# Kernel optimization log

Measured on AMD Instinct MI355X. Metric: run time of the kernel, lower is better.

The kernel has to match this reference:

```python
import jax, jax.numpy as jnp
import numpy as np
import math

M = 0.4      # angular margin
S = 64.0     # scale
K = 0.7      # virtual-prototype damping
START_VP_EPOCH = 4


def _l2norm(v, eps):
    # F.normalize: v / max(||v||_2, eps), row-wise
    n = jnp.sqrt(jnp.sum(v * v, axis=-1, keepdims=True))
    return v / jnp.maximum(n, eps)


def setup_inputs() -> dict:
    key = jax.random.key(0)
    k1, k2, k3, k4 = jax.random.split(key, 4)
    B, D, C = 256, 512, 100000
    return {
        "x": jax.random.normal(k1, (B, D), dtype=jnp.float32),
        "labels": jax.random.randint(k2, (B,), 0, C),
        "weight": jax.random.normal(k3, (C, D), dtype=jnp.float32) * 0.05,
        "queue": jax.random.normal(k4, (C, D), dtype=jnp.float32),
        "epoch": 5,
    }


def reference(x, labels, weight, queue, epoch):
    labels = labels.astype(jnp.int32)
    C = weight.shape[0]

    emb = _l2norm(x, 1e-5)                                   # [B, D]
    cosine = emb @ _l2norm(weight, 1e-5).T                   # [B, C]
    cosine = jnp.clip(cosine, -1.0 + 1e-7, 1.0 - 1e-7)

    # --- update_virtual_prototype (fully detached in the original) ---
    emb_d = jax.lax.stop_gradient(emb)
    q_rows = queue[labels]                                   # [B, D] gather
    # diag(queue[labels] @ emb.T) == rowwise dot (avoid O(B^2) matmul)
    drift = jnp.sum(q_rows * emb_d, axis=1)                  # [B]
    factor = (drift / (1.0 + jnp.abs(drift)))[:, None]       # softsign
    new_rows = _l2norm(factor * q_rows + (1.0 - factor) * emb_d, 1e-12)
    queue = queue.at[labels].set(new_rows)

    if epoch + 1 >= START_VP_EPOCH:
        qn = jax.lax.stop_gradient(_l2norm(queue, 1e-12))    # [C, D]
        vp_sim = emb @ qn.T                                  # [B, C]
        B = vp_sim.shape[0]
        rows = jnp.arange(B)
        diag = vp_sim[rows, labels]
        # v - k * v.detach()  ->  value (1-k)*v, grad passes as identity
        vp_sim = vp_sim.at[rows, labels].set(diag - K * jax.lax.stop_gradient(diag))
        cosine = jnp.concatenate([cosine, vp_sim], axis=0)   # [2B, C]
        labels = jnp.concatenate([labels, labels], axis=0)

    one_hot = labels[:, None] == jnp.arange(C)[None, :]      # [N, C] bool

    sine = jnp.sqrt(jnp.clip(1.0 - cosine * cosine, 0.0, 1.0))
    cosine_m = cosine * math.cos(M) - sine * math.sin(M)
    # characteristic_gradient_detachment: value = cosine_m, grad = d(cosine)
    phi = cosine - jax.lax.stop_gradient(cosine) + jax.lax.stop_gradient(cosine_m)

    logits = jnp.where(one_hot, phi, cosine) * S             # [N, C]

    # EPL loss with one-hot targets
    oh = one_hot.astype(logits.dtype)
    sum_neg = jnp.sum((1.0 - oh) * jnp.exp(logits), axis=1)  # [N]
    sum_pos = jnp.sum(oh * jnp.exp(-logits), axis=1)         # [N]
    loss = jnp.log(1.0 + sum_neg * sum_pos)
    return jnp.mean(loss)
```

## Files before the change

### kernel.cpp

```cpp
#include <hip/hip_runtime.h>
#include <hip/hip_bf16.h>

#define D_DIM 512
#define NROWS 256
#define NT 32
#define KSTEPS 16
#define S_SCALE 64.0f
#define COS_M 0.9210609940028851f
#define SIN_M 0.3894183423086505f

typedef short short8 __attribute__((ext_vector_type(8)));
typedef float f32x4 __attribute__((ext_vector_type(4)));

typedef const __attribute__((address_space(1))) void* gas1_t;
typedef __attribute__((address_space(3))) void* las3_t;

static __device__ __forceinline__ void gload16(const void* g, void* l){
  __builtin_amdgcn_global_load_lds((gas1_t)g, (las3_t)l, 16, 0, 0);
}

static __device__ __forceinline__ short f2bf(float f){
  __hip_bfloat16 h = __float2bfloat16(f);
  return __builtin_bit_cast(short, h);
}

__global__ void k_emb(const float* __restrict__ x, float* __restrict__ emb,
                      short* __restrict__ embA){
  int b = blockIdx.x, t = threadIdx.x;
  float v0 = x[b*D_DIM + t];
  float v1 = x[b*D_DIM + 256 + t];
  __shared__ float red[256];
  red[t] = v0*v0 + v1*v1;
  __syncthreads();
  for (int o=128;o>0;o>>=1){ if(t<o) red[t]+=red[t+o]; __syncthreads(); }
  float inv = 1.0f / fmaxf(sqrtf(red[0]), 1e-5f);
  float e0 = v0*inv, e1 = v1*inv;
  emb[b*D_DIM + t]       = e0;
  emb[b*D_DIM + 256 + t] = e1;
  int rb = b >> 4;
  {
    int d=t; int ks=d>>5, kg=(d>>3)&3, j=d&7;
    int lane=(kg<<4)|(b&15);
    embA[((ks*16+rb)*64+lane)*8+j] = f2bf(e0);
  }
  {
    int d=t+256; int ks=d>>5, kg=(d>>3)&3, j=d&7;
    int lane=(kg<<4)|(b&15);
    embA[((ks*16+rb)*64+lane)*8+j] = f2bf(e1);
  }
}

__global__ void k_init(int* __restrict__ upd, int C){
  int i = blockIdx.x*256 + threadIdx.x;
  if (i < C) upd[i] = -1;
}

__global__ void k_vp(const float* __restrict__ queue, const float* __restrict__ emb,
                     const int* __restrict__ labels, float* __restrict__ newrow,
                     int* __restrict__ upd){
  int b = blockIdx.x, t = threadIdx.x;
  int lab = labels[b];
  const float* q = queue + (size_t)lab * D_DIM;
  float q0=q[t], q1=q[t+256];
  float e0=emb[b*D_DIM+t], e1=emb[b*D_DIM+256+t];
  __shared__ float red[256];
  __shared__ int win;
  red[t] = q0*e0 + q1*e1;
  __syncthreads();
  for (int o=128;o>0;o>>=1){ if(t<o) red[t]+=red[t+o]; __syncthreads(); }
  float drift = red[0];
  float fac = drift / (1.0f + fabsf(drift));
  float v0 = fac*q0 + (1.0f-fac)*e0;
  float v1 = fac*q1 + (1.0f-fac)*e1;
  __syncthreads();
  if (t==0) win = 1;
  red[t] = v0*v0 + v1*v1;
  __syncthreads();
  for (int o=128;o>0;o>>=1){ if(t<o) red[t]+=red[t+o]; __syncthreads(); }
  float inv = 1.0f / fmaxf(sqrtf(red[0]), 1e-12f);
  newrow[b*D_DIM+t]     = v0*inv;
  newrow[b*D_DIM+256+t] = v1*inv;
  if (t > b && labels[t] == lab) win = 0;
  __syncthreads();
  if (t==0 && win) upd[lab] = b;
}

__global__ __launch_bounds__(256,3) void k_main(
    const float* __restrict__ W, const float* __restrict__ Q,
    const short* __restrict__ embA, const float* __restrict__ newrow,
    const int* __restrict__ upd, const int* __restrict__ labels,
    float* __restrict__ partials, float* __restrict__ posval,
    int C, int nwg)
{
  __shared__ __align__(16) char ldsb[4*8192];
  const int wg   = blockIdx.x;
  const int tid  = threadIdx.x;
  const int wave = tid >> 6;
  const int lane = tid & 63;
  const int lcol = lane & 15;
  const int lkg  = lane >> 4;
  const int c0 = wg * NT;
  const int m0 = wave * 64;

  const char* ssrc[2];
  int sdst[2];
#pragma unroll
  for (int i=0;i<2;i++){
    int ch  = wave*2 + i;
    int mat = ch >> 2;
    int r   = (ch&3)*8 + (lane>>3);
    int gs  = (lane&7) ^ (lane>>3);
    int cls = c0 + r; if (cls >= C) cls = C-1;
    const float* rowp;
    if (mat == 0) rowp = W + (size_t)cls * D_DIM;
    else {
      int u = upd[cls];
      rowp = (u >= 0) ? (newrow + (size_t)u * D_DIM) : (Q + (size_t)cls * D_DIM);
    }
    ssrc[i] = (const char*)(rowp + gs*4);
    sdst[i] = ch * 1024;
  }
  __builtin_amdgcn_sched_barrier(0);

  const short8* Af = reinterpret_cast<const short8*>(embA);
  const f32x4 vzero = {0.f,0.f,0.f,0.f};
  f32x4 accW[4][2], accQ[4][2], accNW[2], accNQ[2];
#pragma unroll
  for (int i=0;i<4;i++)
#pragma unroll
    for (int j=0;j<2;j++){ accW[i][j]=vzero; accQ[i][j]=vzero; }
  accNW[0]=vzero; accNW[1]=vzero; accNQ[0]=vzero; accNQ[1]=vzero;

  short8 afc[4], afn[4];
#pragma unroll
  for (int rb=0;rb<4;rb++) afc[rb] = Af[(wave*4 + rb)*64 + lane];
  __builtin_amdgcn_sched_barrier(0);
#pragma unroll
  for (int t=0;t<3;t++){
#pragma unroll
    for (int i=0;i<2;i++)
      gload16(ssrc[i] + t*128, ldsb + t*8192 + sdst[i]);
    __builtin_amdgcn_sched_barrier(0);
  }

#pragma unroll
  for (int ks=0; ks<KSTEPS; ++ks){
    if (ks == 0)            asm volatile("s_waitcnt vmcnt(4)" ::: "memory");
    else if (ks < KSTEPS-2) asm volatile("s_waitcnt vmcnt(2)" ::: "memory");
    else                    asm volatile("s_waitcnt vmcnt(0)" ::: "memory");
    __builtin_amdgcn_s_barrier();
    __builtin_amdgcn_sched_barrier(0);
    if (ks+1 < KSTEPS){
#pragma unroll
      for (int rb=0;rb<4;rb++) afn[rb] = Af[((ks+1)*16 + wave*4 + rb)*64 + lane];
    }
    __builtin_amdgcn_sched_barrier(0);
    if (ks+3 < KSTEPS){
#pragma unroll
      for (int i=0;i<2;i++)
        gload16(ssrc[i] + (ks+3)*128, ldsb + ((ks+3)&3)*8192 + sdst[i]);
    }
    __builtin_amdgcn_sched_barrier(0);

    const char* bb = ldsb + (ks&3)*8192;
#pragma unroll
    for (int cb=0;cb<2;cb++){
      const int row = cb*16 + lcol;
      const int s   = row & 7;
      const int g0  = lkg*2;
      const f32x4 w0 = *(const f32x4*)(bb + row*128 + (((g0  )^s)*16));
      const f32x4 w1 = *(const f32x4*)(bb + row*128 + (((g0+1)^s)*16));
      const f32x4 z0 = *(const f32x4*)(bb + 4096 + row*128 + (((g0  )^s)*16));
      const f32x4 z1 = *(const f32x4*)(bb + 4096 + row*128 + (((g0+1)^s)*16));
      short8 bw, bq;
#pragma unroll
      for (int j=0;j<4;j++){
        bw[j] = f2bf(w0[j]); bw[j+4] = f2bf(w1[j]);
        bq[j] = f2bf(z0[j]); bq[j+4] = f2bf(z1[j]);
      }
      accNW[cb] = __builtin_amdgcn_mfma_f32_16x16x32_bf16(bw, bw, accNW[cb], 0, 0, 0);
      accNQ[cb] = __builtin_amdgcn_mfma_f32_16x16x32_bf16(bq, bq, accNQ[cb], 0, 0, 0);
#pragma unroll
      for (int rb=0;rb<4;rb++)
        accW[rb][cb] = __builtin_amdgcn_mfma_f32_16x16x32_bf16(afc[rb], bw, accW[rb][cb], 0, 0, 0);
#pragma unroll
      for (int rb=0;rb<4;rb++)
        accQ[rb][cb] = __builtin_amdgcn_mfma_f32_16x16x32_bf16(afc[rb], bq, accQ[rb][cb], 0, 0, 0);
    }
#pragma unroll
    for (int rb=0;rb<4;rb++) afc[rb] = afn[rb];
  }

  float winv[2], qinv[2];
#pragma unroll
  for (int cb=0;cb<2;cb++){
    int rsel = lcol & 3;
    float vw = rsel==0?accNW[cb][0]:rsel==1?accNW[cb][1]:rsel==2?accNW[cb][2]:accNW[cb][3];
    float vq = rsel==0?accNQ[cb][0]:rsel==1?accNQ[cb][1]:rsel==2?accNQ[cb][2]:accNQ[cb][3];
    int src = ((lcol>>2)<<4) | lcol;
    float ssW = __shfl(vw, src);
    float ssQ = __shfl(vq, src);
    winv[cb] = 1.0f / fmaxf(sqrtf(ssW), 1e-5f);
    qinv[cb] = 1.0f / fmaxf(sqrtf(ssQ), 1e-12f);
  }

#pragma unroll
  for (int rb=0;rb<4;rb++){
#pragma unroll
    for (int r=0;r<4;r++){
      const int m = m0 + rb*16 + lkg*4 + r;
      const int lab = labels[m];
      float nw = 0.f, nq = 0.f;
#pragma unroll
      for (int cb=0;cb<2;cb++){
        int c = c0 + cb*16 + lcol;
        if (c < C){
          float cw = accW[rb][cb][r] * winv[cb];
          cw = fminf(fmaxf(cw, -1.0f + 1e-7f), 1.0f - 1e-7f);
          float cq = accQ[rb][cb][r] * qinv[cb];
          if (c == lab){
            float sw  = sqrtf(fminf(fmaxf(1.0f - cw*cw, 0.0f), 1.0f));
            float phw = cw*COS_M - sw*SIN_M;
            posval[m] = __expf(-S_SCALE*phw);
            float vq  = 0.3f * cq;
            float sq  = sqrtf(fminf(fmaxf(1.0f - vq*vq, 0.0f), 1.0f));
            float phq = vq*COS_M - sq*SIN_M;
            posval[NROWS + m] = __expf(-S_SCALE*phq);
          } else {
            nw += __expf(S_SCALE*cw);
            nq += __expf(S_SCALE*cq);
          }
        }
      }
#pragma unroll
      for (int msk=1; msk<16; msk<<=1){
        nw += __shfl_xor(nw, msk);
        nq += __shfl_xor(nq, msk);
      }
      if (lcol == 0){
        partials[(size_t)wg*512 + m]       = nw;
        partials[(size_t)wg*512 + 256 + m] = nq;
      }
    }
  }
}

__global__ void k_red(const float* __restrict__ partials, const float* __restrict__ posval,
                      float* __restrict__ lossv, int nwg){
  int n = blockIdx.x, t = threadIdx.x;
  float s = 0.f;
  for (int i=t; i<nwg; i+=256) s += partials[(size_t)i*512 + n];
  __shared__ float red[256];
  red[t] = s; __syncthreads();
  for (int o=128;o>0;o>>=1){ if(t<o) red[t]+=red[t+o]; __syncthreads(); }
  if (t==0) lossv[n] = logf(1.0f + red[0] * posval[n]);
}

__global__ void k_fin(const float* __restrict__ lossv, const int* __restrict__ epoch,
                      float* __restrict__ out){
  int t = threadIdx.x;
  int N = (epoch[0] + 1 >= 4) ? 2*NROWS : NROWS;
  float v = (t < N) ? lossv[t] : 0.f;
  __shared__ float red[512];
  red[t] = v; __syncthreads();
  for (int o=256;o>0;o>>=1){ if(t<o) red[t]+=red[t+o]; __syncthreads(); }
  if (t==0) out[0] = red[0] / (float)N;
}

extern "C" void kernel_launch(void* const* d_in, const int* in_sizes, int n_in,
                              void* d_out, int out_size, void* d_ws, size_t ws_size,
                              hipStream_t stream)
{
  const float* x      = (const float*)d_in[0];
  const int*   labels = (const int*)d_in[1];
  const float* W      = (const float*)d_in[2];
  const float* Q      = (const float*)d_in[3];
  const int*   epoch  = (const int*)d_in[4];
  float* out = (float*)d_out;
  const int C   = in_sizes[2] / D_DIM;
  const int nwg = (C + NT - 1) / NT;

  char* ws = (char*)d_ws;
  float* emb      = (float*)(ws + 0);
  short* embA     = (short*)(ws + 524288);
  float* newrow   = (float*)(ws + 786432);
  int*   upd      = (int*)  (ws + 1310720);
  float* posval   = (float*)(ws + 1712128);
  float* lossv    = (float*)(ws + 1714176);
  float* partials = (float*)(ws + 1716224);

  hipLaunchKernelGGL(k_emb,  dim3(NROWS),       dim3(256), 0, stream, x, emb, embA);
  hipLaunchKernelGGL(k_init, dim3((C+255)/256), dim3(256), 0, stream, upd, C);
  hipLaunchKernelGGL(k_vp,   dim3(NROWS),       dim3(256), 0, stream, Q, emb, labels, newrow, upd);
  hipLaunchKernelGGL(k_main, dim3(nwg),         dim3(256), 0, stream,
                     W, Q, embA, newrow, upd, labels, partials, posval, C, nwg);
  hipLaunchKernelGGL(k_red,  dim3(2*NROWS),     dim3(256), 0, stream, partials, posval, lossv, nwg);
  hipLaunchKernelGGL(k_fin,  dim3(1),           dim3(512), 0, stream, lossv, epoch, out);
}
```

Baseline: 165.8 us.

## Double-buffer A fragments two steps ahead and coalesce partial-sum reduction

The main GEMM loop is manually unrolled through a macro. A-operand register fragments are now double-buffered and prefetched two k-steps ahead, issued after the MFMAs rather than before them, with the vmcnt thresholds adjusted to match. This aims to hide global load latency for the A fragments behind the matrix work, at the cost of more live registers. Separately, the partial-sum reduction kernel now has each block handle 16 output rows with coalesced 16-wide reads instead of one strided column per block, which shrinks the grid from 512 to 32 blocks.

```diff
diff --git a/kernel.cpp b/kernel.cpp
--- a/kernel.cpp
+++ b/kernel.cpp
@@ -131,65 +131,75 @@
     for (int j=0;j<2;j++){ accW[i][j]=vzero; accQ[i][j]=vzero; }
   accNW[0]=vzero; accNW[1]=vzero; accNQ[0]=vzero; accNQ[1]=vzero;
 
-  short8 afc[4], afn[4];
-#pragma unroll
-  for (int rb=0;rb<4;rb++) afc[rb] = Af[(wave*4 + rb)*64 + lane];
-  __builtin_amdgcn_sched_barrier(0);
-#pragma unroll
-  for (int t=0;t<3;t++){
-#pragma unroll
-    for (int i=0;i<2;i++)
-      gload16(ssrc[i] + t*128, ldsb + t*8192 + sdst[i]);
-    __builtin_amdgcn_sched_barrier(0);
-  }
-
-#pragma unroll
-  for (int ks=0; ks<KSTEPS; ++ks){
-    if (ks == 0)            asm volatile("s_waitcnt vmcnt(4)" ::: "memory");
-    else if (ks < KSTEPS-2) asm volatile("s_waitcnt vmcnt(2)" ::: "memory");
-    else                    asm volatile("s_waitcnt vmcnt(0)" ::: "memory");
-    __builtin_amdgcn_s_barrier();
-    __builtin_amdgcn_sched_barrier(0);
-    if (ks+1 < KSTEPS){
-#pragma unroll
-      for (int rb=0;rb<4;rb++) afn[rb] = Af[((ks+1)*16 + wave*4 + rb)*64 + lane];
-    }
-    __builtin_amdgcn_sched_barrier(0);
-    if (ks+3 < KSTEPS){
-#pragma unroll
-      for (int i=0;i<2;i++)
-        gload16(ssrc[i] + (ks+3)*128, ldsb + ((ks+3)&3)*8192 + sdst[i]);
-    }
-    __builtin_amdgcn_sched_barrier(0);
-
-    const char* bb = ldsb + (ks&3)*8192;
-#pragma unroll
-    for (int cb=0;cb<2;cb++){
-      const int row = cb*16 + lcol;
-      const int s   = row & 7;
-      const int g0  = lkg*2;
-      const f32x4 w0 = *(const f32x4*)(bb + row*128 + (((g0  )^s)*16));
-      const f32x4 w1 = *(const f32x4*)(bb + row*128 + (((g0+1)^s)*16));
-      const f32x4 z0 = *(const f32x4*)(bb + 4096 + row*128 + (((g0  )^s)*16));
-      const f32x4 z1 = *(const f32x4*)(bb + 4096 + row*128 + (((g0+1)^s)*16));
-      short8 bw, bq;
-#pragma unroll
-      for (int j=0;j<4;j++){
-        bw[j] = f2bf(w0[j]); bw[j+4] = f2bf(w1[j]);
-        bq[j] = f2bf(z0[j]); bq[j+4] = f2bf(z1[j]);
-      }
-      accNW[cb] = __builtin_amdgcn_mfma_f32_16x16x32_bf16(bw, bw, accNW[cb], 0, 0, 0);
-      accNQ[cb] = __builtin_amdgcn_mfma_f32_16x16x32_bf16(bq, bq, accNQ[cb], 0, 0, 0);
-#pragma unroll
-      for (int rb=0;rb<4;rb++)
-        accW[rb][cb] = __builtin_amdgcn_mfma_f32_16x16x32_bf16(afc[rb], bw, accW[rb][cb], 0, 0, 0);
-#pragma unroll
-      for (int rb=0;rb<4;rb++)
-        accQ[rb][cb] = __builtin_amdgcn_mfma_f32_16x16x32_bf16(afc[rb], bq, accQ[rb][cb], 0, 0, 0);
-    }
-#pragma unroll
-    for (int rb=0;rb<4;rb++) afc[rb] = afn[rb];
-  }
+  short8 af[2][4];
+  gload16(ssrc[0], ldsb + sdst[0]);
+  gload16(ssrc[1], ldsb + sdst[1]);
+  __builtin_amdgcn_sched_barrier(0);
+#pragma unroll
+  for (int rb=0;rb<4;rb++) af[0][rb] = Af[(wave*4 + rb)*64 + lane];
+  __builtin_amdgcn_sched_barrier(0);
+  gload16(ssrc[0] + 128, ldsb + 8192 + sdst[0]);
+  gload16(ssrc[1] + 128, ldsb + 8192 + sdst[1]);
+  gload16(ssrc[0] + 256, ldsb + 16384 + sdst[0]);
+  gload16(ssrc[1] + 256, ldsb + 16384 + sdst[1]);
+  __builtin_amdgcn_sched_barrier(0);
+#pragma unroll
+  for (int rb=0;rb<4;rb++) af[1][rb] = Af[(16 + wave*4 + rb)*64 + lane];
+  __builtin_amdgcn_sched_barrier(0);
+
+#define K_ITER(KS, VM) do {                                                    \
+    asm volatile("s_waitcnt vmcnt(" #VM ")" ::: "memory");                     \
+    __builtin_amdgcn_s_barrier();                                              \
+    __builtin_amdgcn_sched_barrier(0);                                         \
+    if ((KS) + 3 < KSTEPS){                                                    \
+      gload16(ssrc[0] + ((KS)+3)*128, ldsb + (((KS)+3)&3)*8192 + sdst[0]);     \
+      gload16(ssrc[1] + ((KS)+3)*128, ldsb + (((KS)+3)&3)*8192 + sdst[1]);     \
+    }                                                                          \
+    __builtin_amdgcn_sched_barrier(0);                                         \
+    {                                                                          \
+      const char* bb = ldsb + ((KS)&3)*8192;                                   \
+      _Pragma("unroll")                                                        \
+      for (int cb=0;cb<2;cb++){                                                \
+        const int row = cb*16 + lcol;                                          \
+        const int s   = row & 7;                                               \
+        const int g0  = lkg*2;                                                 \
+        const f32x4 w0 = *(const f32x4*)(bb + row*128 + (((g0  )^s)*16));      \
+        const f32x4 w1 = *(const f32x4*)(bb + row*128 + (((g0+1)^s)*16));      \
+        const f32x4 z0 = *(const f32x4*)(bb + 4096 + row*128 + (((g0  )^s)*16));\
+        const f32x4 z1 = *(const f32x4*)(bb + 4096 + row*128 + (((g0+1)^s)*16));\
+        short8 bw, bq;                                                         \
+        _Pragma("unroll")                                                      \
+        for (int j=0;j<4;j++){                                                 \
+          bw[j] = f2bf(w0[j]); bw[j+4] = f2bf(w1[j]);                          \
+          bq[j] = f2bf(z0[j]); bq[j+4] = f2bf(z1[j]);                          \
+        }                                                                      \
+        accNW[cb] = __builtin_amdgcn_mfma_f32_16x16x32_bf16(bw, bw, accNW[cb], 0, 0, 0); \
+        accNQ[cb] = __builtin_amdgcn_mfma_f32_16x16x32_bf16(bq, bq, accNQ[cb], 0, 0, 0); \
+        _Pragma("unroll")                                                      \
+        for (int rb=0;rb<4;rb++)                                               \
+          accW[rb][cb] = __builtin_amdgcn_mfma_f32_16x16x32_bf16(af[(KS)&1][rb], bw, accW[rb][cb], 0, 0, 0); \
+        _Pragma("unroll")                                                      \
+        for (int rb=0;rb<4;rb++)                                               \
+          accQ[rb][cb] = __builtin_amdgcn_mfma_f32_16x16x32_bf16(af[(KS)&1][rb], bq, accQ[rb][cb], 0, 0, 0); \
+      }                                                                        \
+    }                                                                          \
+    __builtin_amdgcn_sched_barrier(0);                                         \
+    if ((KS) + 2 < KSTEPS){                                                    \
+      _Pragma("unroll")                                                        \
+      for (int rb=0;rb<4;rb++)                                                 \
+        af[(KS)&1][rb] = Af[(((KS)+2)*16 + wave*4 + rb)*64 + lane];            \
+    }                                                                          \
+    __builtin_amdgcn_sched_barrier(0);                                         \
+  } while(0)
+
+  K_ITER(0, 8);
+  K_ITER(1, 6);  K_ITER(2, 6);  K_ITER(3, 6);  K_ITER(4, 6);
+  K_ITER(5, 6);  K_ITER(6, 6);  K_ITER(7, 6);  K_ITER(8, 6);
+  K_ITER(9, 6);  K_ITER(10, 6); K_ITER(11, 6); K_ITER(12, 6);
+  K_ITER(13, 6);
+  K_ITER(14, 4);
+  K_ITER(15, 0);
+#undef K_ITER
 
   float winv[2], qinv[2];
 #pragma unroll
@@ -247,13 +257,20 @@
 
 __global__ void k_red(const float* __restrict__ partials, const float* __restrict__ posval,
                       float* __restrict__ lossv, int nwg){
-  int n = blockIdx.x, t = threadIdx.x;
+  int n0 = blockIdx.x * 16;
+  int tx = threadIdx.x & 15, ty = threadIdx.x >> 4;
   float s = 0.f;
-  for (int i=t; i<nwg; i+=256) s += partials[(size_t)i*512 + n];
-  __shared__ float red[256];
-  red[t] = s; __syncthreads();
-  for (int o=128;o>0;o>>=1){ if(t<o) red[t]+=red[t+o]; __syncthreads(); }
-  if (t==0) lossv[n] = logf(1.0f + red[0] * posval[n]);
+  for (int i=ty; i<nwg; i+=16) s += partials[(size_t)i*512 + n0 + tx];
+  __shared__ float red[16][17];
+  red[ty][tx] = s;
+  __syncthreads();
+  if (ty == 0){
+    float acc = 0.f;
+#pragma unroll
+    for (int j=0;j<16;j++) acc += red[j][tx];
+    int n = n0 + tx;
+    lossv[n] = logf(1.0f + acc * posval[n]);
+  }
 }
 
 __global__ void k_fin(const float* __restrict__ lossv, const int* __restrict__ epoch,
@@ -294,6 +311,6 @@
   hipLaunchKernelGGL(k_vp,   dim3(NROWS),       dim3(256), 0, stream, Q, emb, labels, newrow, upd);
   hipLaunchKernelGGL(k_main, dim3(nwg),         dim3(256), 0, stream,
                      W, Q, embA, newrow, upd, labels, partials, posval, C, nwg);
-  hipLaunchKernelGGL(k_red,  dim3(2*NROWS),     dim3(256), 0, stream, partials, posval, lossv, nwg);
+  hipLaunchKernelGGL(k_red,  dim3(32),          dim3(256), 0, stream, partials, posval, lossv, nwg);
   hipLaunchKernelGGL(k_fin,  dim3(1),           dim3(512), 0, stream, lossv, epoch, out);
 }
```

New measurement: 204.6 us. +23.4%, slower.
